# Performance work log

Hardware: AMD Instinct MI355X
Metric: run time of the kernel (lower is better)

Reference implementation:

```python
import jax, jax.numpy as jnp
import numpy as np

P = 16; N_SIDE = 14; N_PATCH = 196
ENC_DIM = 1024; ENC_DEPTH = 2; ENC_HEADS = 16; ENC_DH = 64
DEC_DIM = 512; DEC_DEPTH = 1; DEC_HEADS = 8; DEC_DH = 64
NUM_MASKED = int(0.75 * N_PATCH)  # 147


def _ln(x, s, b):
    m = jnp.mean(x, axis=-1, keepdims=True)
    v = jnp.var(x, axis=-1, keepdims=True)
    return (x - m) * jax.lax.rsqrt(v + 1e-5) * s + b


def _mha(x, Wqkv, Wo, heads, dh):
    B, N, _ = x.shape
    q, k, v = jnp.split(x @ Wqkv, 3, axis=-1)
    rs = lambda t: t.reshape(B, N, heads, dh).transpose(0, 2, 1, 3)
    q, k, v = rs(q), rs(k), rs(v)
    scores = jnp.einsum('bhqd,bhkd->bhqk', q, k) / jnp.sqrt(jnp.float32(dh))
    att = jax.nn.softmax(scores, axis=-1)
    o = jnp.einsum('bhqk,bhkd->bhqd', att, v).transpose(0, 2, 1, 3).reshape(B, N, heads * dh)
    return o @ Wo


def _transformer(x, params, depth, heads, dh, lnfs, lnfb):
    (ln1s, ln1b, Wqkv, Wo, ln2s, ln2b, W1, b1, W2, b2) = params
    for i in range(depth):
        x = x + _mha(_ln(x, ln1s[i], ln1b[i]), Wqkv[i], Wo[i], heads, dh)
        h = jax.nn.gelu(_ln(x, ln2s[i], ln2b[i]) @ W1[i] + b1[i])
        x = x + h @ W2[i] + b2[i]
    return _ln(x, lnfs, lnfb)


def setup_inputs() -> dict:
    key = jax.random.key(0)
    ks = jax.random.split(key, 24)
    B = 64
    w = lambda k, s: (jax.random.normal(k, s, jnp.float32) * 0.02)
    E, IE = ENC_DIM, ENC_HEADS * ENC_DH
    D, ID = DEC_DIM, DEC_HEADS * DEC_DH
    d = {}
    d['images'] = jax.random.normal(ks[0], (B, 224, 224, 3), jnp.float32)
    d['rand'] = jax.random.uniform(ks[1], (B, N_PATCH), dtype=jnp.float32)
    d['patch_W'] = w(ks[2], (P * P * 3, E)); d['patch_b'] = jnp.zeros((E,), jnp.float32)
    d['pos_emb'] = w(ks[3], (N_PATCH, E))
    d['enc_ln1s'] = jnp.ones((ENC_DEPTH, E), jnp.float32); d['enc_ln1b'] = jnp.zeros((ENC_DEPTH, E), jnp.float32)
    d['enc_Wqkv'] = w(ks[4], (ENC_DEPTH, E, 3 * IE)); d['enc_Wo'] = w(ks[5], (ENC_DEPTH, IE, E))
    d['enc_ln2s'] = jnp.ones((ENC_DEPTH, E), jnp.float32); d['enc_ln2b'] = jnp.zeros((ENC_DEPTH, E), jnp.float32)
    d['enc_W1'] = w(ks[6], (ENC_DEPTH, E, 4 * E)); d['enc_b1'] = jnp.zeros((ENC_DEPTH, 4 * E), jnp.float32)
    d['enc_W2'] = w(ks[7], (ENC_DEPTH, 4 * E, E)); d['enc_b2'] = jnp.zeros((ENC_DEPTH, E), jnp.float32)
    d['enc_lnfs'] = jnp.ones((E,), jnp.float32); d['enc_lnfb'] = jnp.zeros((E,), jnp.float32)
    d['e2d_W'] = w(ks[8], (E, D)); d['e2d_b'] = jnp.zeros((D,), jnp.float32)
    d['mask_token'] = w(ks[9], (D,))
    d['dec_pos'] = w(ks[10], (N_PATCH, D))
    d['dec_ln1s'] = jnp.ones((DEC_DEPTH, D), jnp.float32); d['dec_ln1b'] = jnp.zeros((DEC_DEPTH, D), jnp.float32)
    d['dec_Wqkv'] = w(ks[11], (DEC_DEPTH, D, 3 * ID)); d['dec_Wo'] = w(ks[12], (DEC_DEPTH, ID, D))
    d['dec_ln2s'] = jnp.ones((DEC_DEPTH, D), jnp.float32); d['dec_ln2b'] = jnp.zeros((DEC_DEPTH, D), jnp.float32)
    d['dec_W1'] = w(ks[13], (DEC_DEPTH, D, 4 * D)); d['dec_b1'] = jnp.zeros((DEC_DEPTH, 4 * D), jnp.float32)
    d['dec_W2'] = w(ks[14], (DEC_DEPTH, 4 * D, D)); d['dec_b2'] = jnp.zeros((DEC_DEPTH, D), jnp.float32)
    d['dec_lnfs'] = jnp.ones((D,), jnp.float32); d['dec_lnfb'] = jnp.zeros((D,), jnp.float32)
    d['pix_W'] = w(ks[15], (D, E)); d['pix_b'] = jnp.zeros((E,), jnp.float32)  # pixel_dim == encoder_dim per source
    return d


def reference(images, rand, patch_W, patch_b, pos_emb,
              enc_ln1s, enc_ln1b, enc_Wqkv, enc_Wo, enc_ln2s, enc_ln2b,
              enc_W1, enc_b1, enc_W2, enc_b2, enc_lnfs, enc_lnfb,
              e2d_W, e2d_b, mask_token, dec_pos,
              dec_ln1s, dec_ln1b, dec_Wqkv, dec_Wo, dec_ln2s, dec_ln2b,
              dec_W1, dec_b1, dec_W2, dec_b2, dec_lnfs, dec_lnfb,
              pix_W, pix_b):
    B = images.shape[0]
    # patch embed: [B,224,224,3] -> [B,196,768] -> [B,196,1024]
    x = images.reshape(B, N_SIDE, P, N_SIDE, P, 3).transpose(0, 1, 3, 2, 4, 5).reshape(B, N_PATCH, P * P * 3)
    patches = x @ patch_W + patch_b
    tokens = patches + pos_emb
    # random masking via argsort of uniform noise
    order = jnp.argsort(rand, axis=-1)
    m_idx = order[:, :NUM_MASKED]        # [B,147]
    u_idx = order[:, NUM_MASKED:]        # [B,49]
    unmasked = jnp.take_along_axis(tokens, u_idx[:, :, None], axis=1)
    enc_params = (enc_ln1s, enc_ln1b, enc_Wqkv, enc_Wo, enc_ln2s, enc_ln2b, enc_W1, enc_b1, enc_W2, enc_b2)
    encoded = _transformer(unmasked, enc_params, ENC_DEPTH, ENC_HEADS, ENC_DH, enc_lnfs, enc_lnfb)
    dec_tok = encoded @ e2d_W + e2d_b + dec_pos[u_idx]
    mask_toks = mask_token + dec_pos[m_idx]
    bidx = jnp.arange(B)[:, None]
    all_tok = jnp.zeros((B, N_PATCH, DEC_DIM), dec_tok.dtype)
    all_tok = all_tok.at[bidx, u_idx].set(dec_tok)
    all_tok = all_tok.at[bidx, m_idx].set(mask_toks)
    dec_params = (dec_ln1s, dec_ln1b, dec_Wqkv, dec_Wo, dec_ln2s, dec_ln2b, dec_W1, dec_b1, dec_W2, dec_b2)
    decoded = _transformer(all_tok, dec_params, DEC_DEPTH, DEC_HEADS, DEC_DH, dec_lnfs, dec_lnfb)
    pred = jnp.take_along_axis(decoded, m_idx[:, :, None], axis=1) @ pix_W + pix_b
    target = jnp.take_along_axis(patches, m_idx[:, :, None], axis=1)
    return jnp.mean((pred - target) ** 2)
```

## Files before the change

kernel.cpp:

```cpp
#include <hip/hip_runtime.h>

typedef __attribute__((ext_vector_type(8))) __bf16 bf16x8;
typedef __attribute__((ext_vector_type(4))) float f32x4;

#define OFF_PATCH 0ull
#define OFF_X     25690112ull
#define OFF_LN    51380224ull
#define OFF_QKV   64225280ull
#define OFF_HID   103022592ull
#define OFF_WP    154402816ull
#define OFF_ORD   214695936ull
#define OFF_PART  214746112ull

#define WP_PATCH   0ull
#define WP_ENC_QKV 786432ull
#define WP_ENC_WO  7077888ull
#define WP_ENC_W1  9175040ull
#define WP_ENC_W2  17563648ull
#define WP_E2D     25952256ull
#define WP_DEC_QKV 26476544ull
#define WP_DEC_WO  27262976ull
#define WP_DEC_W1  27525120ull
#define WP_DEC_W2  28573696ull
#define WP_PIX     29622272ull

#define OM_BF16 0
#define OM_F32  1
#define OM_ACC  2
#define OM_GELU 3

__device__ __forceinline__ float b2f(unsigned short u) {
    return __uint_as_float(((unsigned int)u) << 16);
}
__device__ __forceinline__ unsigned short f2b(float f) {
    unsigned int x = __float_as_uint(f);
    x += 0x7fffu + ((x >> 16) & 1u);
    return (unsigned short)(x >> 16);
}
__device__ __forceinline__ float gelu_f(float x) {
    float u2 = 1.5957691216057308f * x * (1.f + 0.044715f * x * x);
    return x / (1.f + __expf(-u2));
}
__device__ __forceinline__ void gload16(const void* g, void* l) {
    __builtin_amdgcn_global_load_lds((const __attribute__((address_space(1))) void*)g,
                                     (__attribute__((address_space(3))) void*)l, 16, 0, 0);
}

__global__ __launch_bounds__(256) void pack_w(const float* __restrict__ in,
                                              unsigned short* __restrict__ out, int K, int N) {
    __shared__ float tile[32][33];
    int kt = blockIdx.y * 32, nt = blockIdx.x * 32;
    int tx = threadIdx.x & 31, ty = threadIdx.x >> 5;
#pragma unroll
    for (int i = 0; i < 32; i += 8) tile[ty + i][tx] = in[(size_t)(kt + ty + i) * N + nt + tx];
    __syncthreads();
#pragma unroll
    for (int i = 0; i < 32; i += 8)
        out[(size_t)(nt + ty + i) * K + kt + tx] = f2b(tile[tx][ty + i]);
}

__global__ __launch_bounds__(256) void patchify_kernel(const float* __restrict__ img,
                                                       unsigned short* __restrict__ Xp) {
    const long long total = 12544ll * 768;
    for (long long e = (long long)blockIdx.x * 256 + threadIdx.x; e < total;
         e += (long long)gridDim.x * 256) {
        int row = (int)(e / 768), k = (int)(e % 768);
        int b = row / 196, pi = row % 196;
        int py = pi / 14, px = pi % 14;
        int r = k / 48, rem = k % 48;
        int c = rem / 3, ch = rem % 3;
        long long src = (((long long)(b * 224 + py * 16 + r)) * 224 + (px * 16 + c)) * 3 + ch;
        Xp[e] = f2b(img[src]);
    }
}

template <int BM, int OM, bool ATOMIC>
__global__ __launch_bounds__((BM / 32) * 64) void gemm3(const unsigned short* __restrict__ A,
                                                        const unsigned short* __restrict__ Bt,
                                                        void* __restrict__ Cv,
                                                        const float* __restrict__ bias,
                                                        int M, int N, int K, int Kc) {
    constexpr int WAVES = BM / 32;
    constexpr int BRW = 128 / WAVES;
    constexpr int NIB = BRW / 8;
    __shared__ __align__(16) unsigned short S[BM * 64 + 128 * 64];
    const int tid = threadIdx.x, wave = tid >> 6, lane = tid & 63;
    int nwg = gridDim.x * gridDim.y;
    int orig = blockIdx.y * gridDim.x + blockIdx.x;
    int q = nwg >> 3, r8 = nwg & 7, xcd = orig & 7, off = orig >> 3;
    int wg = (xcd < r8 ? xcd * (q + 1) : r8 * (q + 1) + (xcd - r8) * q) + off;
    const int brow = (wg / gridDim.x) * BM, bcol = (wg % gridDim.x) * 128;
    const int kBeg = blockIdx.z * Kc;
    const int fr = lane & 15, fq = lane >> 4;
    const int wr = (wave >> 1) * 64, wc = (wave & 1) * 64;
    const int lr = lane >> 3;
    const int sca = ((lane & 7) ^ lr) * 8;
    const unsigned short* Agp[4];
#pragma unroll
    for (int i = 0; i < 4; ++i) {
        int r = brow + wave * 32 + i * 8 + lr;
        if (r > M - 1) r = M - 1;
        Agp[i] = A + (size_t)r * K + kBeg + sca;
    }
    const unsigned short* Bgp[NIB];
#pragma unroll
    for (int i = 0; i < NIB; ++i) {
        int r = bcol + wave * BRW + i * 8 + lr;
        Bgp[i] = Bt + (size_t)r * K + kBeg + sca;
    }

    f32x4 acc[4][4];
#pragma unroll
    for (int m = 0; m < 4; ++m)
#pragma unroll
        for (int n = 0; n < 4; ++n) acc[m][n] = (f32x4){0.f, 0.f, 0.f, 0.f};

    const char* lds = (const char*)S;
    const int sw = (fr & 7) << 4;
    const int a0 = (wr + fr) * 128 + ((fq * 16) ^ sw);
    const int b0 = BM * 128 + (wc + fr) * 128 + ((fq * 16) ^ sw);

    const int nt = Kc >> 6;
    for (int t = 0; t < nt; ++t) {
        __syncthreads();
        const int k0 = t << 6;
#pragma unroll
        for (int i = 0; i < 4; ++i)
            gload16(Agp[i] + k0, S + (wave * 32 + i * 8) * 64);
#pragma unroll
        for (int i = 0; i < NIB; ++i)
            gload16(Bgp[i] + k0, S + BM * 64 + (wave * BRW + i * 8) * 64);
        __syncthreads();
        __builtin_amdgcn_s_setprio(1);
#pragma unroll
        for (int kk = 0; kk < 2; ++kk) {
            const int kx = kk * 64;
            bf16x8 af[4], bf[4];
#pragma unroll
            for (int m = 0; m < 4; ++m)
                af[m] = *(const bf16x8*)(lds + ((a0 ^ kx) + m * 2048));
#pragma unroll
            for (int n = 0; n < 4; ++n)
                bf[n] = *(const bf16x8*)(lds + ((b0 ^ kx) + n * 2048));
#pragma unroll
            for (int m = 0; m < 4; ++m)
#pragma unroll
                for (int n = 0; n < 4; ++n)
                    acc[m][n] = __builtin_amdgcn_mfma_f32_16x16x32_bf16(af[m], bf[n],
                                                                       acc[m][n], 0, 0, 0);
        }
        __builtin_amdgcn_s_setprio(0);
    }

    const bool addBias = (bias != nullptr) && (kBeg == 0);
#pragma unroll
    for (int m = 0; m < 4; ++m) {
        int rb = brow + wr + m * 16 + fq * 4;
#pragma unroll
        for (int r = 0; r < 4; ++r) {
            int row = rb + r;
            if (row < M) {
#pragma unroll
                for (int n = 0; n < 4; ++n) {
                    int col = bcol + wc + n * 16 + fr;
                    float v = acc[m][n][r];
                    if (addBias) v += bias[col];
                    size_t o = (size_t)row * N + col;
                    if constexpr (ATOMIC) atomicAdd((float*)Cv + o, v);
                    else if constexpr (OM == OM_BF16) ((unsigned short*)Cv)[o] = f2b(v);
                    else if constexpr (OM == OM_F32) ((float*)Cv)[o] = v;
                    else if constexpr (OM == OM_ACC) ((float*)Cv)[o] += v;
                    else ((unsigned short*)Cv)[o] = f2b(gelu_f(v));
                }
            }
        }
    }
}

template <int N, int H, int NW>
__global__ __launch_bounds__(NW * 64) void attn_mfma(const unsigned short* __restrict__ qkv,
                                                     unsigned short* __restrict__ out) {
    constexpr int Npad = ((N + 31) / 32) * 32;
    constexpr int NT = Npad / 16;
    constexpr int KS = Npad / 32;
    constexpr int PS = Npad + 8;
    constexpr int SQ = 3 * H * 64, SO = H * 64;
    __shared__ __align__(16) unsigned short Kl[Npad * 64];
    __shared__ __align__(16) unsigned short Vt[64 * PS];
    __shared__ __align__(16) unsigned short Pl[NW * 16 * PS];
    const int b = blockIdx.x / H, h = blockIdx.x % H;
    const unsigned short* base = qkv + (size_t)b * N * SQ;
    const int qoff = h * 64, koff = (H + h) * 64, voff = (2 * H + h) * 64;
    const int tid = threadIdx.x, wave = tid >> 6, lane = tid & 63;
    const int fr = lane & 15, fq = lane >> 4;

    for (int idx = tid; idx < Npad * 8; idx += NW * 64) {
        int row = idx >> 3, ch = idx & 7;
        uint4 v = {0u, 0u, 0u, 0u};
        if (row < N) v = *(const uint4*)(base + (size_t)row * SQ + koff + ch * 8);
        *(uint4*)((char*)Kl + row * 128 + ((ch * 16) ^ ((row & 7) << 4))) = v;
    }
    for (int idx = tid; idx < Npad * 32; idx += NW * 64) {
        int key = idx >> 5, d2 = (idx & 31) * 2;
        unsigned int v = 0;
        if (key < N) v = *(const unsigned int*)(base + (size_t)key * SQ + voff + d2);
        Vt[d2 * PS + key] = (unsigned short)(v & 0xffffu);
        Vt[(d2 + 1) * PS + key] = (unsigned short)(v >> 16);
    }
    __syncthreads();

    unsigned short* pw = Pl + wave * 16 * PS;
    for (int qt = wave; qt < NT; qt += NW) {
        const int q0 = qt * 16;
        int qr = q0 + fr;
        if (qr > N - 1) qr = N - 1;
        const unsigned short* qp = base + (size_t)qr * SQ + qoff + fq * 8;
        bf16x8 aq0 = *(const bf16x8*)qp;
        bf16x8 aq1 = *(const bf16x8*)(qp + 32);
        f32x4 sa[NT];
#pragma unroll
        for (int ct = 0; ct < NT; ++ct) sa[ct] = (f32x4){0.f, 0.f, 0.f, 0.f};
#pragma unroll
        for (int ct = 0; ct < NT; ++ct) {
            const char* kb = (const char*)Kl + (ct * 16 + fr) * 128;
            bf16x8 kf0 = *(const bf16x8*)(kb + ((fq * 16) ^ ((fr & 7) << 4)));
            bf16x8 kf1 = *(const bf16x8*)(kb + ((64 + fq * 16) ^ ((fr & 7) << 4)));
            sa[ct] = __builtin_amdgcn_mfma_f32_16x16x32_bf16(aq0, kf0, sa[ct], 0, 0, 0);
            sa[ct] = __builtin_amdgcn_mfma_f32_16x16x32_bf16(aq1, kf1, sa[ct], 0, 0, 0);
        }
        float mrow[4] = {-3e38f, -3e38f, -3e38f, -3e38f};
#pragma unroll
        for (int ct = 0; ct < NT; ++ct) {
            bool ok = (ct * 16 + fr) < N;
#pragma unroll
            for (int r = 0; r < 4; ++r) {
                float s = ok ? sa[ct][r] * 0.125f : -3e38f;
                sa[ct][r] = s;
                mrow[r] = fmaxf(mrow[r], s);
            }
        }
#pragma unroll
        for (int off = 1; off <= 8; off <<= 1)
#pragma unroll
            for (int r = 0; r < 4; ++r) mrow[r] = fmaxf(mrow[r], __shfl_xor(mrow[r], off));
        float ssum[4] = {0.f, 0.f, 0.f, 0.f};
#pragma unroll
        for (int ct = 0; ct < NT; ++ct)
#pragma unroll
            for (int r = 0; r < 4; ++r) {
                float p = __expf(sa[ct][r] - mrow[r]);
                sa[ct][r] = p;
                ssum[r] += p;
            }
#pragma unroll
        for (int off = 1; off <= 8; off <<= 1)
#pragma unroll
            for (int r = 0; r < 4; ++r) ssum[r] += __shfl_xor(ssum[r], off);
#pragma unroll
        for (int ct = 0; ct < NT; ++ct)
#pragma unroll
            for (int r = 0; r < 4; ++r)
                pw[(fq * 4 + r) * PS + ct * 16 + fr] = f2b(sa[ct][r]);
        f32x4 oa[4];
#pragma unroll
        for (int vt = 0; vt < 4; ++vt) oa[vt] = (f32x4){0.f, 0.f, 0.f, 0.f};
#pragma unroll
        for (int ks = 0; ks < KS; ++ks) {
            bf16x8 pa = *(const bf16x8*)(pw + fr * PS + ks * 32 + fq * 8);
#pragma unroll
            for (int vt = 0; vt < 4; ++vt) {
                bf16x8 vf = *(const bf16x8*)(&Vt[(vt * 16 + fr) * PS + ks * 32 + fq * 8]);
                oa[vt] = __builtin_amdgcn_mfma_f32_16x16x32_bf16(pa, vf, oa[vt], 0, 0, 0);
            }
        }
        float inv[4];
#pragma unroll
        for (int r = 0; r < 4; ++r) inv[r] = 1.f / ssum[r];
#pragma unroll
        for (int vt = 0; vt < 4; ++vt)
#pragma unroll
            for (int r = 0; r < 4; ++r) {
                int q = q0 + fq * 4 + r;
                if (q < N)
                    out[((size_t)b * N + q) * SO + h * 64 + vt * 16 + fr] =
                        f2b(oa[vt][r] * inv[r]);
            }
    }
}

__global__ __launch_bounds__(256) void argsort_kernel(const float* __restrict__ rnd,
                                                      int* __restrict__ ord) {
    __shared__ float vals[196];
    int b = blockIdx.x, t = threadIdx.x;
    if (t < 196) vals[t] = rnd[b * 196 + t];
    __syncthreads();
    if (t < 196) {
        float v = vals[t];
        int rank = 0;
        for (int j = 0; j < 196; ++j) {
            float vj = vals[j];
            rank += (vj < v) || (vj == v && j < t);
        }
        ord[b * 196 + rank] = t;
    }
}

__global__ __launch_bounds__(256) void gather_unmasked(const unsigned short* __restrict__ patches,
                                                       const float* __restrict__ pos,
                                                       const int* __restrict__ ord,
                                                       float* __restrict__ xe) {
    int row = blockIdx.x;
    int b = row / 49, i = row % 49;
    int src = ord[b * 196 + 147 + i];
    const unsigned short* pr = patches + ((size_t)(b * 196 + src) << 10);
    const float* pe = pos + ((size_t)src << 10);
    float* o = xe + ((size_t)row << 10);
    int d = threadIdx.x * 4;
    ushort4 pv = *(const ushort4*)(pr + d);
    float4 p4 = *(const float4*)(pe + d);
    float4 r;
    r.x = b2f(pv.x) + p4.x; r.y = b2f(pv.y) + p4.y;
    r.z = b2f(pv.z) + p4.z; r.w = b2f(pv.w) + p4.w;
    *(float4*)(o + d) = r;
}

template <int L>
__global__ __launch_bounds__(256) void ln_kernel(const float* __restrict__ x,
                                                 unsigned short* __restrict__ y,
                                                 const float* __restrict__ sw,
                                                 const float* __restrict__ bw) {
    __shared__ float red[8];
    const int tid = threadIdx.x;
    const float* xr = x + (size_t)blockIdx.x * L;
    float sum = 0.f, sq = 0.f;
    for (int i = tid * 4; i < L; i += 1024) {
        float4 v = *(const float4*)(xr + i);
        sum += v.x + v.y + v.z + v.w;
        sq += v.x * v.x + v.y * v.y + v.z * v.z + v.w * v.w;
    }
    for (int off = 32; off; off >>= 1) {
        sum += __shfl_xor(sum, off);
        sq += __shfl_xor(sq, off);
    }
    int wave = tid >> 6, lane = tid & 63;
    if (lane == 0) { red[wave] = sum; red[4 + wave] = sq; }
    __syncthreads();
    float ts = red[0] + red[1] + red[2] + red[3];
    float tq = red[4] + red[5] + red[6] + red[7];
    float mean = ts / L;
    float inv = rsqrtf(tq / L - mean * mean + 1e-5f);
    unsigned short* yr = y + (size_t)blockIdx.x * L;
    for (int i = tid * 4; i < L; i += 1024) {
        float4 v = *(const float4*)(xr + i);
        float4 s4 = *(const float4*)(sw + i);
        float4 b4 = *(const float4*)(bw + i);
        ushort4 o;
        o.x = f2b((v.x - mean) * inv * s4.x + b4.x);
        o.y = f2b((v.y - mean) * inv * s4.y + b4.y);
        o.z = f2b((v.z - mean) * inv * s4.z + b4.z);
        o.w = f2b((v.w - mean) * inv * s4.w + b4.w);
        *(ushort4*)(yr + i) = o;
    }
}

__global__ __launch_bounds__(256) void scatter_tokens(const float* __restrict__ dec_tok,
                                                      const float* __restrict__ dec_pos,
                                                      const float* __restrict__ mask_tok,
                                                      const int* __restrict__ ord,
                                                      float* __restrict__ all_tok) {
    int e = blockIdx.x;
    int b = e / 196, i = e % 196;
    int idx = ord[e];
    float* o = all_tok + ((size_t)(b * 196 + idx)) * 512;
    const float* dp = dec_pos + (size_t)idx * 512;
    int d = threadIdx.x * 4;
    if (d < 512) {
        float4 dv = *(const float4*)(dp + d);
        float4 sv;
        if (i < 147) sv = *(const float4*)(mask_tok + d);
        else sv = *(const float4*)(dec_tok + ((size_t)(b * 49 + (i - 147))) * 512 + d);
        float4 r = {sv.x + dv.x, sv.y + dv.y, sv.z + dv.z, sv.w + dv.w};
        *(float4*)(o + d) = r;
    }
}

__global__ __launch_bounds__(256) void gather_masked(const unsigned short* __restrict__ x,
                                                     const int* __restrict__ ord,
                                                     unsigned short* __restrict__ gm) {
    int r = blockIdx.x;
    int b = r / 147, j = r % 147;
    int idx = ord[b * 196 + j];
    const unsigned short* src = x + ((size_t)(b * 196 + idx)) * 512;
    unsigned short* o = gm + (size_t)r * 512;
    int d = threadIdx.x * 4;
    if (d < 512) *(ushort4*)(o + d) = *(const ushort4*)(src + d);
}

__global__ __launch_bounds__(256) void loss_partial(const float* __restrict__ pred,
                                                    const unsigned short* __restrict__ patches,
                                                    const int* __restrict__ ord,
                                                    float* __restrict__ part) {
    __shared__ float red[8];
    float local = 0.f;
    const long long total = 9633792ll;
    for (long long e = (long long)blockIdx.x * 256 + threadIdx.x; e < total; e += 4096ll * 256) {
        int r = (int)(e >> 10), d = (int)(e & 1023);
        int b = r / 147, j = r % 147;
        int idx = ord[b * 196 + j];
        float t = b2f(patches[(((size_t)(b * 196 + idx)) << 10) + d]);
        float df = pred[e] - t;
        local += df * df;
    }
    for (int off = 32; off; off >>= 1) local += __shfl_xor(local, off);
    int wave = threadIdx.x >> 6, lane = threadIdx.x & 63;
    if (lane == 0) red[wave] = local;
    __syncthreads();
    if (threadIdx.x == 0) part[blockIdx.x] = red[0] + red[1] + red[2] + red[3];
}

__global__ __launch_bounds__(256) void loss_final(const float* __restrict__ part,
                                                  float* __restrict__ out) {
    __shared__ float red[8];
    float local = 0.f;
    for (int i = threadIdx.x; i < 4096; i += 256) local += part[i];
    for (int off = 32; off; off >>= 1) local += __shfl_xor(local, off);
    int wave = threadIdx.x >> 6, lane = threadIdx.x & 63;
    if (lane == 0) red[wave] = local;
    __syncthreads();
    if (threadIdx.x == 0) out[0] = (red[0] + red[1] + red[2] + red[3]) / 9633792.0f;
}

extern "C" void kernel_launch(void* const* d_in, const int* in_sizes, int n_in, void* d_out,
                              int out_size, void* d_ws, size_t ws_size, hipStream_t stream) {
    const float* images = (const float*)d_in[0];
    const float* rnd = (const float*)d_in[1];
    const float* patch_W = (const float*)d_in[2];
    const float* patch_b = (const float*)d_in[3];
    const float* pos_emb = (const float*)d_in[4];
    const float* enc_ln1s = (const float*)d_in[5];
    const float* enc_ln1b = (const float*)d_in[6];
    const float* enc_Wqkv = (const float*)d_in[7];
    const float* enc_Wo = (const float*)d_in[8];
    const float* enc_ln2s = (const float*)d_in[9];
    const float* enc_ln2b = (const float*)d_in[10];
    const float* enc_W1 = (const float*)d_in[11];
    const float* enc_b1 = (const float*)d_in[12];
    const float* enc_W2 = (const float*)d_in[13];
    const float* enc_b2 = (const float*)d_in[14];
    const float* enc_lnfs = (const float*)d_in[15];
    const float* enc_lnfb = (const float*)d_in[16];
    const float* e2d_W = (const float*)d_in[17];
    const float* e2d_b = (const float*)d_in[18];
    const float* mask_tok = (const float*)d_in[19];
    const float* dec_pos = (const float*)d_in[20];
    const float* dec_ln1s = (const float*)d_in[21];
    const float* dec_ln1b = (const float*)d_in[22];
    const float* dec_Wqkv = (const float*)d_in[23];
    const float* dec_Wo = (const float*)d_in[24];
    const float* dec_ln2s = (const float*)d_in[25];
    const float* dec_ln2b = (const float*)d_in[26];
    const float* dec_W1 = (const float*)d_in[27];
    const float* dec_b1 = (const float*)d_in[28];
    const float* dec_W2 = (const float*)d_in[29];
    const float* dec_b2 = (const float*)d_in[30];
    const float* dec_lnfs = (const float*)d_in[31];
    const float* dec_lnfb = (const float*)d_in[32];
    const float* pix_W = (const float*)d_in[33];
    const float* pix_b = (const float*)d_in[34];

    char* ws = (char*)d_ws;
    unsigned short* patches = (unsigned short*)(ws + OFF_PATCH);
    float* Rx = (float*)(ws + OFF_X);
    unsigned short* Rln = (unsigned short*)(ws + OFF_LN);
    unsigned short* RqkvB = (unsigned short*)(ws + OFF_QKV);
    float* RqkvF = (float*)(ws + OFF_QKV);
    unsigned short* Rhid = (unsigned short*)(ws + OFF_HID);
    unsigned short* wp = (unsigned short*)(ws + OFF_WP);
    int* ord = (int*)(ws + OFF_ORD);
    float* part = (float*)(ws + OFF_PART);
    float* out = (float*)d_out;

    auto PACK = [&](const float* src, size_t wpo, int K, int N) {
        pack_w<<<dim3(N / 32, K / 32), 256, 0, stream>>>(src, wp + wpo, K, N);
    };
    PACK(patch_W, WP_PATCH, 768, 1024);
    for (int l = 0; l < 2; ++l) {
        PACK(enc_Wqkv + (size_t)l * 1024 * 3072, WP_ENC_QKV + (size_t)l * 3145728, 1024, 3072);
        PACK(enc_Wo + (size_t)l * 1024 * 1024, WP_ENC_WO + (size_t)l * 1048576, 1024, 1024);
        PACK(enc_W1 + (size_t)l * 1024 * 4096, WP_ENC_W1 + (size_t)l * 4194304, 1024, 4096);
        PACK(enc_W2 + (size_t)l * 4096 * 1024, WP_ENC_W2 + (size_t)l * 4194304, 4096, 1024);
    }
    PACK(e2d_W, WP_E2D, 1024, 512);
    PACK(dec_Wqkv, WP_DEC_QKV, 512, 1536);
    PACK(dec_Wo, WP_DEC_WO, 512, 512);
    PACK(dec_W1, WP_DEC_W1, 512, 2048);
    PACK(dec_W2, WP_DEC_W2, 2048, 512);
    PACK(pix_W, WP_PIX, 512, 1024);

    auto GEMM = [&](int om, const unsigned short* A, size_t wpo, void* C, const float* bias,
                    int M, int N, int K, int S, bool small) {
        const unsigned short* Bt = wp + wpo;
        int Kc = K / S;
        if (!small) {
            dim3 g(N / 128, (M + 255) / 256, S);
            if (S > 1) gemm3<256, OM_ACC, true><<<g, 512, 0, stream>>>(A, Bt, C, bias, M, N, K, Kc);
            else if (om == OM_BF16) gemm3<256, OM_BF16, false><<<g, 512, 0, stream>>>(A, Bt, C, bias, M, N, K, Kc);
            else if (om == OM_F32) gemm3<256, OM_F32, false><<<g, 512, 0, stream>>>(A, Bt, C, bias, M, N, K, Kc);
            else if (om == OM_ACC) gemm3<256, OM_ACC, false><<<g, 512, 0, stream>>>(A, Bt, C, bias, M, N, K, Kc);
            else gemm3<256, OM_GELU, false><<<g, 512, 0, stream>>>(A, Bt, C, bias, M, N, K, Kc);
        } else {
            dim3 g(N / 128, (M + 127) / 128, S);
            if (S > 1) gemm3<128, OM_ACC, true><<<g, 256, 0, stream>>>(A, Bt, C, bias, M, N, K, Kc);
            else if (om == OM_BF16) gemm3<128, OM_BF16, false><<<g, 256, 0, stream>>>(A, Bt, C, bias, M, N, K, Kc);
            else if (om == OM_F32) gemm3<128, OM_F32, false><<<g, 256, 0, stream>>>(A, Bt, C, bias, M, N, K, Kc);
            else if (om == OM_ACC) gemm3<128, OM_ACC, false><<<g, 256, 0, stream>>>(A, Bt, C, bias, M, N, K, Kc);
            else gemm3<128, OM_GELU, false><<<g, 256, 0, stream>>>(A, Bt, C, bias, M, N, K, Kc);
        }
    };

    patchify_kernel<<<4096, 256, 0, stream>>>(images, Rhid);
    GEMM(OM_BF16, Rhid, WP_PATCH, patches, patch_b, 12544, 1024, 768, 1, false);
    argsort_kernel<<<64, 256, 0, stream>>>(rnd, ord);
    gather_unmasked<<<3136, 256, 0, stream>>>(patches, pos_emb, ord, Rx);

    for (int l = 0; l < 2; ++l) {
        ln_kernel<1024><<<3136, 256, 0, stream>>>(Rx, Rln, enc_ln1s + l * 1024,
                                                  enc_ln1b + l * 1024);
        GEMM(OM_BF16, Rln, WP_ENC_QKV + (size_t)l * 3145728, RqkvB, nullptr, 3136, 3072, 1024,
             1, false);
        attn_mfma<49, 16, 4><<<64 * 16, 256, 0, stream>>>(RqkvB, Rhid);
        GEMM(OM_ACC, Rhid, WP_ENC_WO + (size_t)l * 1048576, Rx, nullptr, 3136, 1024, 1024, 2,
             false);
        ln_kernel<1024><<<3136, 256, 0, stream>>>(Rx, Rln, enc_ln2s + l * 1024,
                                                  enc_ln2b + l * 1024);
        GEMM(OM_GELU, Rln, WP_ENC_W1 + (size_t)l * 4194304, Rhid, enc_b1 + l * 4096, 3136,
             4096, 1024, 1, false);
        GEMM(OM_ACC, Rhid, WP_ENC_W2 + (size_t)l * 4194304, Rx, enc_b2 + l * 1024, 3136, 1024,
             4096, 4, false);
    }
    ln_kernel<1024><<<3136, 256, 0, stream>>>(Rx, Rln, enc_lnfs, enc_lnfb);

    GEMM(OM_F32, Rln, WP_E2D, RqkvF, e2d_b, 3136, 512, 1024, 1, true);
    scatter_tokens<<<12544, 256, 0, stream>>>(RqkvF, dec_pos, mask_tok, ord, Rx);

    ln_kernel<512><<<12544, 256, 0, stream>>>(Rx, Rln, dec_ln1s, dec_ln1b);
    GEMM(OM_BF16, Rln, WP_DEC_QKV, RqkvB, nullptr, 12544, 1536, 512, 1, false);
    attn_mfma<196, 8, 8><<<64 * 8, 512, 0, stream>>>(RqkvB, Rhid);
    GEMM(OM_ACC, Rhid, WP_DEC_WO, Rx, nullptr, 12544, 512, 512, 1, false);
    ln_kernel<512><<<12544, 256, 0, stream>>>(Rx, Rln, dec_ln2s, dec_ln2b);
    GEMM(OM_GELU, Rln, WP_DEC_W1, Rhid, dec_b1, 12544, 2048, 512, 1, false);
    GEMM(OM_ACC, Rhid, WP_DEC_W2, Rx, dec_b2, 12544, 512, 2048, 2, false);
    ln_kernel<512><<<12544, 256, 0, stream>>>(Rx, Rln, dec_lnfs, dec_lnfb);

    gather_masked<<<9408, 256, 0, stream>>>(Rln, ord, Rhid);
    GEMM(OM_F32, Rhid, WP_PIX, RqkvF, pix_b, 9408, 1024, 512, 1, false);
    loss_partial<<<4096, 256, 0, stream>>>(RqkvF, patches, ord, part);
    loss_final<<<1, 256, 0, stream>>>(part, out);
}
```

Before: 852.1 us.

## Add 256x256-tile GEMM with interleaved prefetch and use it for large GEMMs

Adds a new gemm8 kernel that computes 256x256 output tiles with 8 waves. It double-buffers 64-wide K slices in 128 KB of LDS using XOR-swizzled direct global-to-LDS loads, and issues the next tile's loads in stages interleaved with the MFMA phases, raising MFMA priority around the math. The patch, encoder QKV/W1/W2 and decoder QKV/W1/W2 GEMMs switch to it, while the others keep the old 256x128 kernel. The larger tile increases operand reuse and arithmetic intensity, at the cost of fewer workgroups, lower occupancy and possible tail imbalance on the smaller GEMMs.

Result: slower. 1.017 ms (+19.4%).

```diff
diff --git a/kernel.cpp b/kernel.cpp
--- a/kernel.cpp
+++ b/kernel.cpp
@@ -44,6 +44,11 @@
 __device__ __forceinline__ void gload16(const void* g, void* l) {
     __builtin_amdgcn_global_load_lds((const __attribute__((address_space(1))) void*)g,
                                      (__attribute__((address_space(3))) void*)l, 16, 0, 0);
+}
+__device__ __forceinline__ void fbar() {
+    asm volatile("" ::: "memory");
+    __builtin_amdgcn_s_barrier();
+    asm volatile("" ::: "memory");
 }
 
 __global__ __launch_bounds__(256) void pack_w(const float* __restrict__ in,
@@ -71,6 +76,136 @@
         int c = rem / 3, ch = rem % 3;
         long long src = (((long long)(b * 224 + py * 16 + r)) * 224 + (px * 16 + c)) * 3 + ch;
         Xp[e] = f2b(img[src]);
+    }
+}
+
+template <int OM, bool ATOMIC>
+__global__ __launch_bounds__(512) void gemm8(const unsigned short* __restrict__ A,
+                                             const unsigned short* __restrict__ Bt,
+                                             void* __restrict__ Cv,
+                                             const float* __restrict__ bias,
+                                             int M, int N, int K, int Kc) {
+    __shared__ __align__(16) unsigned short S[65536];
+    const int tid = threadIdx.x, w = tid >> 6, lane = tid & 63;
+    const int wm = w >> 2, wn = w & 3;
+    const int fr = lane & 15, fq = lane >> 4;
+    const int lr = lane >> 3;
+    int nwg = gridDim.x * gridDim.y;
+    int orig = blockIdx.y * gridDim.x + blockIdx.x;
+    int q8 = nwg >> 3, r8 = nwg & 7, xcd = orig & 7, off = orig >> 3;
+    int wg = (xcd < r8 ? xcd * (q8 + 1) : r8 * (q8 + 1) + (xcd - r8) * q8) + off;
+    const int brow = (wg / gridDim.x) * 256, bcol = (wg % gridDim.x) * 256;
+    const int kBeg = blockIdx.z * Kc;
+    const int sca = ((lane & 7) ^ lr) * 8;
+    const unsigned short* Aq[4];
+#pragma unroll
+    for (int q = 0; q < 4; ++q) {
+        int r = brow + q * 64 + w * 8 + lr;
+        if (r > M - 1) r = M - 1;
+        Aq[q] = A + (size_t)r * K + kBeg + sca;
+    }
+    const unsigned short* Bc[4];
+#pragma unroll
+    for (int c = 0; c < 4; ++c) {
+        int r = bcol + c * 64 + w * 8 + lr;
+        Bc[c] = Bt + (size_t)r * K + kBeg + sca;
+    }
+    const int nt = Kc >> 6;
+
+    auto stA = [&](int q, int t) {
+        gload16(Aq[q] + (t << 6), S + (t & 1) * 32768 + (q * 64 + w * 8) * 64);
+    };
+    auto stB = [&](int c, int t) {
+        gload16(Bc[c] + (t << 6), S + (t & 1) * 32768 + 16384 + (c * 64 + w * 8) * 64);
+    };
+#pragma unroll
+    for (int q = 0; q < 4; ++q) { stA(q, 0); stB(q, 0); }
+#pragma unroll
+    for (int c = 0; c < 3; ++c) { stA(c, 1); stB(c, 1); }
+    asm volatile("s_waitcnt vmcnt(6)" ::: "memory");
+    fbar();
+
+    f32x4 acc[8][4];
+#pragma unroll
+    for (int m = 0; m < 8; ++m)
+#pragma unroll
+        for (int n = 0; n < 4; ++n) acc[m][n] = (f32x4){0.f, 0.f, 0.f, 0.f};
+
+    const char* lds = (const char*)S;
+    const int sw = (fr & 7) << 4;
+    const int rA = wm * 32 + fr;
+    const int rB = wn * 64 + fr;
+    bf16x8 bfr[4][2];
+
+    for (int t = 0; t < nt; ++t) {
+        const int sb = (t & 1) << 16;
+#pragma unroll
+        for (int p = 0; p < 4; ++p) {
+            bf16x8 af[2][2];
+#pragma unroll
+            for (int mm = 0; mm < 2; ++mm)
+#pragma unroll
+                for (int kk = 0; kk < 2; ++kk) {
+                    int row = p * 64 + rA + mm * 16;
+                    af[mm][kk] =
+                        *(const bf16x8*)(lds + sb + row * 128 + ((kk * 64 + fq * 16) ^ sw));
+                }
+            if (p == 0) {
+#pragma unroll
+                for (int n = 0; n < 4; ++n)
+#pragma unroll
+                    for (int kk = 0; kk < 2; ++kk) {
+                        int row = rB + n * 16;
+                        bfr[n][kk] = *(const bf16x8*)(lds + sb + 32768 + row * 128 +
+                                                      ((kk * 64 + fq * 16) ^ sw));
+                    }
+                if (t + 1 < nt) { stA(3, t + 1); stB(3, t + 1); }
+            } else {
+                if (t + 2 < nt) { stA(p - 1, t + 2); stB(p - 1, t + 2); }
+            }
+            fbar();
+            __builtin_amdgcn_s_setprio(1);
+#pragma unroll
+            for (int mm = 0; mm < 2; ++mm)
+#pragma unroll
+                for (int n = 0; n < 4; ++n)
+#pragma unroll
+                    for (int kk = 0; kk < 2; ++kk)
+                        acc[p * 2 + mm][n] = __builtin_amdgcn_mfma_f32_16x16x32_bf16(
+                            af[mm][kk], bfr[n][kk], acc[p * 2 + mm][n], 0, 0, 0);
+            __builtin_amdgcn_s_setprio(0);
+            if (p == 3 && t < nt - 1) {
+                if (t < nt - 2)
+                    asm volatile("s_waitcnt vmcnt(6)" ::: "memory");
+                else
+                    asm volatile("s_waitcnt vmcnt(0)" ::: "memory");
+            }
+            fbar();
+        }
+    }
+
+    const bool addBias = (bias != nullptr) && (kBeg == 0);
+#pragma unroll
+    for (int m = 0; m < 8; ++m) {
+        int rb = brow + (m >> 1) * 64 + wm * 32 + (m & 1) * 16 + fq * 4;
+#pragma unroll
+        for (int r = 0; r < 4; ++r) {
+            int row = rb + r;
+            if (row < M) {
+#pragma unroll
+                for (int n = 0; n < 4; ++n) {
+                    int col = bcol + wn * 64 + n * 16 + fr;
+                    float v = acc[m][n][r];
+                    if (addBias) v += bias[col];
+                    size_t o = (size_t)row * N + col;
+                    if constexpr (ATOMIC) atomicAdd((float*)Cv + o, v);
+                    else if constexpr (OM == OM_BF16) ((unsigned short*)Cv)[o] = f2b(v);
+                    else if constexpr (OM == OM_F32) ((float*)Cv)[o] = v;
+                    else if constexpr (OM == OM_ACC) ((float*)Cv)[o] += v;
+                    else ((unsigned short*)Cv)[o] = f2b(gelu_f(v));
+                }
+            }
+        }
     }
 }
 
@@ -497,8 +632,19 @@
     PACK(dec_W2, WP_DEC_W2, 2048, 512);
     PACK(pix_W, WP_PIX, 512, 1024);
 
-    auto GEMM = [&](int om, const unsigned short* A, size_t wpo, void* C, const float* bias,
-                    int M, int N, int K, int S, bool small) {
+    auto GEMM8 = [&](int om, const unsigned short* A, size_t wpo, void* C, const float* bias,
+                     int M, int N, int K, int S) {
+        const unsigned short* Bt = wp + wpo;
+        dim3 g(N / 256, (M + 255) / 256, S);
+        int Kc = K / S;
+        if (S > 1) gemm8<OM_ACC, true><<<g, 512, 0, stream>>>(A, Bt, C, bias, M, N, K, Kc);
+        else if (om == OM_BF16) gemm8<OM_BF16, false><<<g, 512, 0, stream>>>(A, Bt, C, bias, M, N, K, Kc);
+        else if (om == OM_F32) gemm8<OM_F32, false><<<g, 512, 0, stream>>>(A, Bt, C, bias, M, N, K, Kc);
+        else if (om == OM_ACC) gemm8<OM_ACC, false><<<g, 512, 0, stream>>>(A, Bt, C, bias, M, N, K, Kc);
+        else gemm8<OM_GELU, false><<<g, 512, 0, stream>>>(A, Bt, C, bias, M, N, K, Kc);
+    };
+    auto GEMM3 = [&](int om, const unsigned short* A, size_t wpo, void* C, const float* bias,
+                     int M, int N, int K, int S, bool small) {
         const unsigned short* Bt = wp + wpo;
         int Kc = K / S;
         if (!small) {
@@ -519,41 +665,41 @@
     };
 
     patchify_kernel<<<4096, 256, 0, stream>>>(images, Rhid);
-    GEMM(OM_BF16, Rhid, WP_PATCH, patches, patch_b, 12544, 1024, 768, 1, false);
+    GEMM8(OM_BF16, Rhid, WP_PATCH, patches, patch_b, 12544, 1024, 768, 1);
     argsort_kernel<<<64, 256, 0, stream>>>(rnd, ord);
     gather_unmasked<<<3136, 256, 0, stream>>>(patches, pos_emb, ord, Rx);
 
     for (int l = 0; l < 2; ++l) {
         ln_kernel<1024><<<3136, 256, 0, stream>>>(Rx, Rln, enc_ln1s + l * 1024,
                                                   enc_ln1b + l * 1024);
-        GEMM(OM_BF16, Rln, WP_ENC_QKV + (size_t)l * 3145728, RqkvB, nullptr, 3136, 3072, 1024,
-             1, false);
+        GEMM8(OM_BF16, Rln, WP_ENC_QKV + (size_t)l * 3145728, RqkvB, nullptr, 3136, 3072,
+              1024, 1);
         attn_mfma<49, 16, 4><<<64 * 16, 256, 0, stream>>>(RqkvB, Rhid);
-        GEMM(OM_ACC, Rhid, WP_ENC_WO + (size_t)l * 1048576, Rx, nullptr, 3136, 1024, 1024, 2,
-             false);
+        GEMM3(OM_ACC, Rhid, WP_ENC_WO + (size_t)l * 1048576, Rx, nullptr, 3136, 1024, 1024, 2,
+              false);
         ln_kernel<1024><<<3136, 256, 0, stream>>>(Rx, Rln, enc_ln2s + l * 1024,
                                                   enc_ln2b + l * 1024);
-        GEMM(OM_GELU, Rln, WP_ENC_W1 + (size_t)l * 4194304, Rhid, enc_b1 + l * 4096, 3136,
-             4096, 1024, 1, false);
-        GEMM(OM_ACC, Rhid, WP_ENC_W2 + (size_t)l * 4194304, Rx, enc_b2 + l * 1024, 3136, 1024,
-             4096, 4, false);
+        GEMM8(OM_GELU, Rln, WP_ENC_W1 + (size_t)l * 4194304, Rhid, enc_b1 + l * 4096, 3136,
+              4096, 1024, 1);
+        GEMM8(OM_ACC, Rhid, WP_ENC_W2 + (size_t)l * 4194304, Rx, enc_b2 + l * 1024, 3136,
+              1024, 4096, 4);
     }
     ln_kernel<1024><<<3136, 256, 0, stream>>>(Rx, Rln, enc_lnfs, enc_lnfb);
 
-    GEMM(OM_F32, Rln, WP_E2D, RqkvF, e2d_b, 3136, 512, 1024, 1, true);
+    GEMM3(OM_F32, Rln, WP_E2D, RqkvF, e2d_b, 3136, 512, 1024, 1, true);
     scatter_tokens<<<12544, 256, 0, stream>>>(RqkvF, dec_pos, mask_tok, ord, Rx);
 
     ln_kernel<512><<<12544, 256, 0, stream>>>(Rx, Rln, dec_ln1s, dec_ln1b);
-    GEMM(OM_BF16, Rln, WP_DEC_QKV, RqkvB, nullptr, 12544, 1536, 512, 1, false);
+    GEMM8(OM_BF16, Rln, WP_DEC_QKV, RqkvB, nullptr, 12544, 1536, 512, 1);
     attn_mfma<196, 8, 8><<<64 * 8, 512, 0, stream>>>(RqkvB, Rhid);
-    GEMM(OM_ACC, Rhid, WP_DEC_WO, Rx, nullptr, 12544, 512, 512, 1, false);
+    GEMM3(OM_ACC, Rhid, WP_DEC_WO, Rx, nullptr, 12544, 512, 512, 1, false);
     ln_kernel<512><<<12544, 256, 0, stream>>>(Rx, Rln, dec_ln2s, dec_ln2b);
-    GEMM(OM_GELU, Rln, WP_DEC_W1, Rhid, dec_b1, 12544, 2048, 512, 1, false);
-    GEMM(OM_ACC, Rhid, WP_DEC_W2, Rx, dec_b2, 12544, 512, 2048, 2, false);
+    GEMM8(OM_GELU, Rln, WP_DEC_W1, Rhid, dec_b1, 12544, 2048, 512, 1);
+    GEMM8(OM_ACC, Rhid, WP_DEC_W2, Rx, dec_b2, 12544, 512, 2048, 2);
     ln_kernel<512><<<12544, 256, 0, stream>>>(Rx, Rln, dec_lnfs, dec_lnfb);
 
     gather_masked<<<9408, 256, 0, stream>>>(Rln, ord, Rhid);
-    GEMM(OM_F32, Rhid, WP_PIX, RqkvF, pix_b, 9408, 1024, 512, 1, false);
+    GEMM3(OM_F32, Rhid, WP_PIX, RqkvF, pix_b, 9408, 1024, 512, 1, false);
     loss_partial<<<4096, 256, 0, stream>>>(RqkvF, patches, ord, part);
     loss_final<<<1, 256, 0, stream>>>(part, out);
 }
```
